# Kernel tuning notes

Measured on AMD Instinct MI355X. Metric: run time of the kernel, lower is better.

## Reference

```python
import jax, jax.numpy as jnp
import numpy as np

B = 64          # num_graphs per batch
ADJ = 1000      # adj_shape (nodes per graph)
N = B * ADJ     # total nodes
E = 1 << 20     # edges
M = 32000       # selected (batch, node) pairs
D_IN = 128
D_OUT = 128


def setup_inputs() -> dict:
    key = jax.random.key(0)
    ks = jax.random.split(key, 12)
    inp = {
        "x0": jax.random.normal(ks[0], (N, D_IN), jnp.float32),
        "x1": jax.random.normal(ks[1], (N, D_IN), jnp.float32),
        "edge_index": jax.random.randint(ks[2], (2, E), 0, N, jnp.int64),
        "b_idx0": jax.random.randint(ks[3], (M,), 0, B, jnp.int64),
        "n_idx0": jax.random.randint(ks[4], (M,), 0, ADJ, jnp.int64),
        "b_idx1": jax.random.randint(ks[5], (M,), 0, B, jnp.int64),
        "n_idx1": jax.random.randint(ks[6], (M,), 0, ADJ, jnp.int64),
        "W1": jax.random.normal(ks[7], (D_IN, D_IN), jnp.float32) / np.sqrt(D_IN),
        "b1": jnp.zeros((D_IN,), jnp.float32),
        "W2": jax.random.normal(ks[8], (D_IN, D_IN), jnp.float32) / np.sqrt(D_IN),
        "b2": jnp.zeros((D_IN,), jnp.float32),
        "Wl": jax.random.normal(ks[9], (D_IN, D_OUT), jnp.float32) / np.sqrt(D_IN),
        "bl": jnp.zeros((D_OUT,), jnp.float32),
        "Wfi": jax.random.normal(ks[10], (D_IN, D_OUT), jnp.float32) / np.sqrt(D_IN),
        "bfi": jnp.zeros((D_OUT,), jnp.float32),
    }
    return inp


def _gnn_layer(h, edge_index, W, b):
    # GCN-style message passing: gather source features, scatter-sum to dst,
    # then linear project.  h: [N, d]
    msgs = h[edge_index[0]]                                    # [E, d] gather
    agg = jax.ops.segment_sum(msgs, edge_index[1], num_segments=N)  # [N, d]
    return agg @ W + b


def reference(x0, x1, edge_index, b_idx0, n_idx0, b_idx1, n_idx1,
              W1, b1, W2, b2, Wl, bl, Wfi, bfi):
    # branch i == 0: raw features -> 2D gather -> fc_in
    d0 = x0.reshape(B, ADJ, -1)[b_idx0, n_idx0]                # [M, D_IN]
    d0 = d0 @ Wfi + bfi                                        # [M, D_OUT]

    # branch i == 1 (observ=True): gnn1 -> gnn2 -> 2D gather -> linear
    # (dropout omitted for deterministic reference; p=0.2 at train time)
    h = _gnn_layer(x1, edge_index, W1, b1)
    h = _gnn_layer(h, edge_index, W2, b2)
    d1 = h.reshape(B, ADJ, -1)[b_idx1, n_idx1]                 # [M, D_IN]
    d1 = d1 @ Wl + bl                                          # [M, D_OUT]

    return jnp.stack([d0, d1])                                 # [2, M, D_OUT]
```

## Files before the change

### kernel.cpp

```cpp
#include <hip/hip_runtime.h>
#include <hip/hip_bf16.h>


#define B_    64
#define ADJ_  1000
#define N_    64000
#define E_    (1 << 20)
#define M_    32000
#define DV    128
#define CAP   64
#define CHUNKS 4096
#define EPB   (E_ / CHUNKS)
#define AGUNROLL 24

typedef __attribute__((ext_vector_type(8))) short short8v;
typedef __attribute__((ext_vector_type(4))) float float4v;

__device__ __forceinline__ float u2f(unsigned int u) {
  union { unsigned int i; float f; } x; x.i = u; return x.f;
}
__device__ __forceinline__ unsigned short f2bf(float f) {
  union { float f; unsigned int i; } x; x.f = f;
  unsigned int r = x.i + 0x7fffu + ((x.i >> 16) & 1u);
  return (unsigned short)(r >> 16);
}
__device__ __forceinline__ unsigned int pack_bf2(float a, float b) {
  __hip_bfloat162 h = __float22bfloat162_rn(float2{a, b});
  union { __hip_bfloat162 h; unsigned int u; } c; c.h = h;
  return c.u;
}

__device__ __forceinline__ int frag_addr(int k, int n) {
  return ((((n >> 4) * 4 + (k >> 5)) * 64 + ((k >> 3) & 3) * 16 + (n & 15)) << 3)
       + (k & 7);
}

__global__ __launch_bounds__(256)
void prep_k(const float* __restrict__ W1, const float* __restrict__ Wfi,
            const float* __restrict__ W2, const float* __restrict__ Wl,
            const float* __restrict__ b2, const float* __restrict__ bl,
            unsigned short* __restrict__ Wbf, float* __restrict__ bc,
            int* __restrict__ counts) {
  int b = blockIdx.x, t = threadIdx.x;
  if (b < 16) {
    const float* W = (b < 8) ? W1 : Wfi;
    unsigned short* out = Wbf + ((b < 8) ? 0 : 16384);
    int base = (b & 7) * 2048 + t * 8;
    float4 f0 = *(const float4*)(W + base);
    float4 f1 = *(const float4*)(W + base + 4);
    float v[8] = {f0.x, f0.y, f0.z, f0.w, f1.x, f1.y, f1.z, f1.w};
#pragma unroll
    for (int u = 0; u < 8; u++) {
      int g = base + u;
      out[frag_addr(g >> 7, g & 127)] = f2bf(v[u]);
    }
  } else if (b < 32) {
    unsigned short* out = Wbf + 2 * 16384;
    int g0 = (b - 16) * 1024 + t * 4;
    int k = g0 >> 7, n = g0 & 127;
    float4 acc = {0.f, 0.f, 0.f, 0.f};
    for (int j = 0; j < 128; j++) {
      float w2 = W2[k * 128 + j];
      float4 wl = *(const float4*)(Wl + j * 128 + n);
      acc.x += w2 * wl.x; acc.y += w2 * wl.y;
      acc.z += w2 * wl.z; acc.w += w2 * wl.w;
    }
    out[frag_addr(k, n + 0)] = f2bf(acc.x);
    out[frag_addr(k, n + 1)] = f2bf(acc.y);
    out[frag_addr(k, n + 2)] = f2bf(acc.z);
    out[frag_addr(k, n + 3)] = f2bf(acc.w);
  } else {
    if (t < 128) {
      float acc = bl[t];
      for (int k = 0; k < 128; k++) acc += b2[k] * Wl[k * 128 + t];
      bc[t] = acc;
    }
  }
  for (int i = b * 256 + t; i < N_; i += 33 * 256) counts[i] = 0;
}

__device__ __forceinline__ void fill_once(const int* __restrict__ ei,
                                          int* __restrict__ counts,
                                          unsigned short* __restrict__ bucket,
                                          int c) {
  int e = c * EPB + (int)threadIdx.x;
  int d = ei[E_ + e];
  int s = ei[e];
  int pos = atomicAdd(&counts[d], 1);
  if (pos < CAP)
    bucket[(size_t)d * CAP + pos] = (unsigned short)s;
}

template<bool GATHER, bool ABF16, bool OUTBF16, bool HASBIAS>
__device__ __forceinline__ void gemm_tile(const void* __restrict__ in,
                                          const unsigned short* __restrict__ Wbf,
                                          const float* __restrict__ bias,
                                          void* __restrict__ out_, int tile,
                                          const int* __restrict__ bidx,
                                          const int* __restrict__ nidx,
                                          unsigned short* __restrict__ Bs) {
  int tid  = threadIdx.x;
  int lane = tid & 63;
  int wv   = tid >> 6;
  int m    = lane & 15;
  int q    = lane >> 4;
  int rbase = tile * 64 + wv * 16;
  int r     = rbase + m;

  const short8v* Wv  = (const short8v*)Wbf;
  short8v*       Bsv = (short8v*)Bs;

  short8v w[4];
#pragma unroll
  for (int i = 0; i < 4; i++) w[i] = Wv[tid + i * 256];

  size_t ir;
  if (GATHER) ir = (size_t)bidx[r] * ADJ_ + nidx[r];
  else        ir = (size_t)r;

  short8v af[4];
  if (ABF16) {
    const unsigned short* arow = (const unsigned short*)in + ir * DV;
#pragma unroll
    for (int kc = 0; kc < 4; kc++)
      af[kc] = *(const short8v*)(arow + kc * 32 + q * 8);
  } else {
    const float* arow = (const float*)in + ir * DV;
#pragma unroll
    for (int kc = 0; kc < 4; kc++) {
      const float4* p = (const float4*)(arow + kc * 32 + q * 8);
      float4 f0 = p[0], f1 = p[1];
      union { short8v s; unsigned int u[4]; } t;
      t.u[0] = pack_bf2(f0.x, f0.y);
      t.u[1] = pack_bf2(f0.z, f0.w);
      t.u[2] = pack_bf2(f1.x, f1.y);
      t.u[3] = pack_bf2(f1.z, f1.w);
      af[kc] = t.s;
    }
  }

#pragma unroll
  for (int i = 0; i < 4; i++) Bsv[tid + i * 256] = w[i];
  __syncthreads();

  float4v acc[8];
#pragma unroll
  for (int nb = 0; nb < 8; nb++) acc[nb] = (float4v){0.f, 0.f, 0.f, 0.f};

#pragma unroll
  for (int i = 0; i < 4; i++) w[i] = Wv[1024 + tid + i * 256];

#pragma unroll
  for (int nb = 0; nb < 4; nb++)
#pragma unroll
    for (int kc = 0; kc < 4; kc++) {
      short8v bf = Bsv[(nb * 4 + kc) * 64 + lane];
      acc[nb] = __builtin_amdgcn_mfma_f32_16x16x32_bf16(af[kc], bf, acc[nb], 0, 0, 0);
    }
  __syncthreads();
#pragma unroll
  for (int i = 0; i < 4; i++) Bsv[tid + i * 256] = w[i];
  __syncthreads();
#pragma unroll
  for (int nb = 4; nb < 8; nb++)
#pragma unroll
    for (int kc = 0; kc < 4; kc++) {
      short8v bf = Bsv[((nb - 4) * 4 + kc) * 64 + lane];
      acc[nb] = __builtin_amdgcn_mfma_f32_16x16x32_bf16(af[kc], bf, acc[nb], 0, 0, 0);
    }

#pragma unroll
  for (int nb = 0; nb < 8; nb++) {
    float bvn = HASBIAS ? bias[nb * 16 + m] : 0.f;
    int col = nb * 16 + m;
#pragma unroll
    for (int i = 0; i < 4; i++) {
      int row = rbase + q * 4 + i;
      float v = acc[nb][i] + bvn;
      if (OUTBF16) ((unsigned short*)out_)[(size_t)row * DV + col] = f2bf(v);
      else         ((float*)out_)[(size_t)row * DV + col] = v;
    }
  }
}

__global__ __launch_bounds__(256)
void k1_fused(const int* __restrict__ ei, int* __restrict__ counts,
              unsigned short* __restrict__ bucket,
              const float* __restrict__ x1, const unsigned short* __restrict__ Wbf,
              unsigned int* __restrict__ t_bf,
              const float* __restrict__ x0, const float* __restrict__ bfi,
              float* __restrict__ out0,
              const int* __restrict__ b0, const int* __restrict__ n0i) {
  __shared__ unsigned short Bs[8192];
  int g = blockIdx.x / 11, rem = blockIdx.x % 11;
  if (rem < 8) { fill_once(ei, counts, bucket, g * 8 + rem); return; }
  int o = g * 3 + rem - 8;
  if (o < 1000)
    gemm_tile<false, false, true, false>(x1, Wbf, nullptr, t_bf, o, nullptr, nullptr, Bs);
  else if (o < 1500)
    gemm_tile<true, false, false, true>(x0, Wbf + 16384, bfi, out0, o - 1000, b0, n0i, Bs);
}

template<bool GATHER, bool ABF16, bool OUTBF16, bool HASBIAS>
__global__ __launch_bounds__(256)
void gemm_k(const void* __restrict__ in, const unsigned short* __restrict__ Wbf,
            const float* __restrict__ bias, void* __restrict__ out_,
            const int* __restrict__ bidx, const int* __restrict__ nidx) {
  __shared__ unsigned short Bs[8192];
  gemm_tile<GATHER, ABF16, OUTBF16, HASBIAS>(in, Wbf, bias, out_, blockIdx.x, bidx, nidx, Bs);
}

template<bool OUTBF16, bool SEL>
__global__ __launch_bounds__(256)
void aggregate_k(const uint2* __restrict__ x,
                 const int* __restrict__ counts,
                 const unsigned int* __restrict__ bucket,
                 const float* __restrict__ bias, void* __restrict__ out_,
                 const int* __restrict__ bidx, const int* __restrict__ nidx) {
  int wave = (blockIdx.x * 256 + threadIdx.x) >> 6;
  int lane = threadIdx.x & 63;
  int l5   = lane & 31;
  int r    = wave * 2 + (lane >> 5);
  int node = SEL ? (bidx[r] * ADJ_ + nidx[r]) : r;
  int cnt  = counts[node]; cnt = min(cnt, CAP);
  unsigned int mp = bucket[node * 32 + l5];

  float4 acc;
  if (bias) acc = ((const float4*)bias)[l5];
  else      acc = float4{0.f, 0.f, 0.f, 0.f};

#define SLOT_C(i)                                                            \
  ((int)((((unsigned int)__shfl((int)mp, ((i) >> 1) | (lane & 32), 64))      \
          >> (((i) & 1) * 16)) & 0xffffu))

  uint2 uu[AGUNROLL];
#pragma unroll
  for (int i = 0; i < AGUNROLL; i++)
    if (i < cnt) {
      int s = SLOT_C(i);
      uu[i] = x[(size_t)s * 32 + l5];
    }
#pragma unroll
  for (int i = 0; i < AGUNROLL; i++)
    if (i < cnt) {
      acc.x += u2f(uu[i].x << 16);
      acc.y += u2f(uu[i].x & 0xffff0000u);
      acc.z += u2f(uu[i].y << 16);
      acc.w += u2f(uu[i].y & 0xffff0000u);
    }
  for (int d = AGUNROLL; d < cnt; d++) {
    unsigned int v = (unsigned int)__shfl((int)mp, (d >> 1) | (lane & 32), 64);
    int s = (int)((v >> ((d & 1) * 16)) & 0xffffu);
    uint2 u = x[(size_t)s * 32 + l5];
    acc.x += u2f(u.x << 16);
    acc.y += u2f(u.x & 0xffff0000u);
    acc.z += u2f(u.y << 16);
    acc.w += u2f(u.y & 0xffff0000u);
  }
#undef SLOT_C

  if (OUTBF16) {
    uint2 p; p.x = pack_bf2(acc.x, acc.y); p.y = pack_bf2(acc.z, acc.w);
    ((uint2*)out_)[(size_t)r * 32 + l5] = p;
  } else {
    ((float4*)out_)[(size_t)r * 32 + l5] = acc;
  }
}

extern "C" void kernel_launch(void* const* d_in, const int* in_sizes, int n_in,
                              void* d_out, int out_size, void* d_ws, size_t ws_size,
                              hipStream_t stream) {
  const float* x0  = (const float*)d_in[0];
  const float* x1  = (const float*)d_in[1];
  const int*   ei  = (const int*)  d_in[2];
  const int*   b0  = (const int*)  d_in[3];
  const int*   n0i = (const int*)  d_in[4];
  const int*   b1  = (const int*)  d_in[5];
  const int*   n1i = (const int*)  d_in[6];
  const float* W1  = (const float*)d_in[7];
  const float* bb1 = (const float*)d_in[8];
  const float* W2  = (const float*)d_in[9];
  const float* bb2 = (const float*)d_in[10];
  const float* Wl  = (const float*)d_in[11];
  const float* bl  = (const float*)d_in[12];
  const float* Wfi = (const float*)d_in[13];
  const float* bfi = (const float*)d_in[14];
  float* out = (float*)d_out;

  unsigned int*   t_bf   = (unsigned int*)d_ws;
  unsigned int*   sel_bf = t_bf;
  unsigned int*   h_bf   = t_bf + (size_t)N_ * 64;
  int*            counts = (int*)(h_bf + (size_t)N_ * 64);
  unsigned short* bucket = (unsigned short*)(counts + N_);
  unsigned short* Wbf    = bucket + (size_t)N_ * CAP;
  float*          bc     = (float*)(Wbf + 3 * 16384);

  prep_k<<<33, 256, 0, stream>>>(W1, Wfi, W2, Wl, bb2, bl, Wbf, bc, counts);

  k1_fused<<<5632, 256, 0, stream>>>(ei, counts, bucket, x1, Wbf, t_bf,
                                     x0, bfi, out, b0, n0i);

  aggregate_k<true, false><<<N_ / 8, 256, 0, stream>>>((const uint2*)t_bf, counts,
                                                       (const unsigned int*)bucket,
                                                       bb1, h_bf, nullptr, nullptr);
  aggregate_k<true, true><<<M_ / 8, 256, 0, stream>>>((const uint2*)h_bf, counts,
                                                      (const unsigned int*)bucket,
                                                      nullptr, sel_bf, b1, n1i);
  gemm_k<false, true, false, true><<<M_ / 64, 256, 0, stream>>>(sel_bf, Wbf + 2 * 16384,
                                                                bc, out + (size_t)M_ * DV,
                                                                nullptr, nullptr);
}
```

Before: 261.8 us.

## Fuse selected-row aggregation with final linear projection via MFMA

```diff
diff --git a/kernel.cpp b/kernel.cpp
--- a/kernel.cpp
+++ b/kernel.cpp
@@ -201,15 +201,6 @@
     gemm_tile<true, false, false, true>(x0, Wbf + 16384, bfi, out0, o - 1000, b0, n0i, Bs);
 }
 
-template<bool GATHER, bool ABF16, bool OUTBF16, bool HASBIAS>
-__global__ __launch_bounds__(256)
-void gemm_k(const void* __restrict__ in, const unsigned short* __restrict__ Wbf,
-            const float* __restrict__ bias, void* __restrict__ out_,
-            const int* __restrict__ bidx, const int* __restrict__ nidx) {
-  __shared__ unsigned short Bs[8192];
-  gemm_tile<GATHER, ABF16, OUTBF16, HASBIAS>(in, Wbf, bias, out_, blockIdx.x, bidx, nidx, Bs);
-}
-
 template<bool OUTBF16, bool SEL>
 __global__ __launch_bounds__(256)
 void aggregate_k(const uint2* __restrict__ x,
@@ -264,6 +255,117 @@
     ((uint2*)out_)[(size_t)r * 32 + l5] = p;
   } else {
     ((float4*)out_)[(size_t)r * 32 + l5] = acc;
+  }
+}
+
+__global__ __launch_bounds__(256)
+void aggmm_k(const uint4* __restrict__ x,
+             const int* __restrict__ counts,
+             const unsigned short* __restrict__ bucket,
+             const unsigned short* __restrict__ WbfC,
+             const float* __restrict__ bc, float* __restrict__ out1,
+             const int* __restrict__ bidx, const int* __restrict__ nidx) {
+  __shared__ unsigned short Bs[8192];
+  int tid  = threadIdx.x;
+  int lane = tid & 63;
+  int wv   = tid >> 6;
+  int m    = lane & 15;
+  int q    = lane >> 4;
+  int rbase = blockIdx.x * 64 + wv * 16;
+  int r     = rbase + m;
+
+  const short8v* Wv  = (const short8v*)WbfC;
+  short8v*       Bsv = (short8v*)Bs;
+  short8v w[4];
+#pragma unroll
+  for (int i = 0; i < 4; i++) w[i] = Wv[tid + i * 256];
+
+  int node = bidx[r] * ADJ_ + nidx[r];
+  int cnt  = counts[node]; cnt = min(cnt, CAP);
+  const unsigned short* brow = bucket + (size_t)node * CAP;
+
+  int maxc = cnt;
+#pragma unroll
+  for (int off = 1; off < 16; off <<= 1)
+    maxc = max(maxc, __shfl_xor(maxc, off, 64));
+
+  float acc[4][8];
+#pragma unroll
+  for (int kc = 0; kc < 4; kc++)
+#pragma unroll
+    for (int j = 0; j < 8; j++) acc[kc][j] = 0.f;
+
+#define ACCU(kc, u) do {                                                \
+    acc[kc][0] += u2f((u).x << 16); acc[kc][1] += u2f((u).x & 0xffff0000u); \
+    acc[kc][2] += u2f((u).y << 16); acc[kc][3] += u2f((u).y & 0xffff0000u); \
+    acc[kc][4] += u2f((u).z << 16); acc[kc][5] += u2f((u).z & 0xffff0000u); \
+    acc[kc][6] += u2f((u).w << 16); acc[kc][7] += u2f((u).w & 0xffff0000u); \
+  } while (0)
+
+#pragma unroll 2
+  for (int i = 0; i < maxc; i++) {
+    if (i < cnt) {
+      int s = (int)brow[i];
+      const uint4* src = x + (size_t)s * 16 + q;
+      uint4 u0 = src[0];
+      uint4 u1 = src[4];
+      uint4 u2 = src[8];
+      uint4 u3 = src[12];
+      ACCU(0, u0); ACCU(1, u1); ACCU(2, u2); ACCU(3, u3);
+    }
+  }
+#undef ACCU
+
+  short8v af[4];
+#pragma unroll
+  for (int kc = 0; kc < 4; kc++) {
+    union { short8v s; unsigned int u[4]; } t;
+    t.u[0] = pack_bf2(acc[kc][0], acc[kc][1]);
+    t.u[1] = pack_bf2(acc[kc][2], acc[kc][3]);
+    t.u[2] = pack_bf2(acc[kc][4], acc[kc][5]);
+    t.u[3] = pack_bf2(acc[kc][6], acc[kc][7]);
+    af[kc] = t.s;
+  }
+
+#pragma unroll
+  for (int i = 0; i < 4; i++) Bsv[tid + i * 256] = w[i];
+  __syncthreads();
+
+  float4v accm[8];
+#pragma unroll
+  for (int nb = 0; nb < 8; nb++) accm[nb] = (float4v){0.f, 0.f, 0.f, 0.f};
+
+#pragma unroll
+  for (int i = 0; i < 4; i++) w[i] = Wv[1024 + tid + i * 256];
+
+#pragma unroll
+  for (int nb = 0; nb < 4; nb++)
+#pragma unroll
+    for (int kc = 0; kc < 4; kc++) {
+      short8v bf = Bsv[(nb * 4 + kc) * 64 + lane];
+      accm[nb] = __builtin_amdgcn_mfma_f32_16x16x32_bf16(af[kc], bf, accm[nb], 0, 0, 0);
+    }
+  __syncthreads();
+#pragma unroll
+  for (int i = 0; i < 4; i++) Bsv[tid + i * 256] = w[i];
+  __syncthreads();
+#pragma unroll
+  for (int nb = 4; nb < 8; nb++)
+#pragma unroll
+    for (int kc = 0; kc < 4; kc++) {
+      short8v bf = Bsv[((nb - 4) * 4 + kc) * 64 + lane];
+      accm[nb] = __builtin_amdgcn_mfma_f32_16x16x32_bf16(af[kc], bf, accm[nb], 0, 0, 0);
+    }
+
+#pragma unroll
+  for (int nb = 0; nb < 8; nb++) {
+    int col = nb * 16 + m;
+    float bvn = bc[col];
+#pragma unroll
+    for (int i = 0; i < 4; i++) {
+      int row = rbase + q * 4 + i;
+      out1[(size_t)row * DV + col] = accm[nb][i] + bvn;
+    }
   }
 }
 
@@ -288,7 +390,6 @@
   float* out = (float*)d_out;
 
   unsigned int*   t_bf   = (unsigned int*)d_ws;
-  unsigned int*   sel_bf = t_bf;
   unsigned int*   h_bf   = t_bf + (size_t)N_ * 64;
   int*            counts = (int*)(h_bf + (size_t)N_ * 64);
   unsigned short* bucket = (unsigned short*)(counts + N_);
@@ -303,10 +404,7 @@
   aggregate_k<true, false><<<N_ / 8, 256, 0, stream>>>((const uint2*)t_bf, counts,
                                                        (const unsigned int*)bucket,
                                                        bb1, h_bf, nullptr, nullptr);
-  aggregate_k<true, true><<<M_ / 8, 256, 0, stream>>>((const uint2*)h_bf, counts,
-                                                      (const unsigned int*)bucket,
-                                                      nullptr, sel_bf, b1, n1i);
-  gemm_k<false, true, false, true><<<M_ / 64, 256, 0, stream>>>(sel_bf, Wbf + 2 * 16384,
-                                                                bc, out + (size_t)M_ * DV,
-                                                                nullptr, nullptr);
-}
+  aggmm_k<<<M_ / 64, 256, 0, stream>>>((const uint4*)h_bf, counts, bucket,
+                                       Wbf + 2 * 16384, bc, out + (size_t)M_ * DV,
+                                       b1, n1i);
+}
```

Measured after the change: 261.6 us. About the same (-0.1%).
